# Optimization experiments

Hardware: AMD Instinct MI355X
Metric: run time of the kernel (lower is better)

The kernel has to match this reference:

```python
import jax, jax.numpy as jnp
import numpy as np

OS = 14            # output_size
GRID = 2           # ceil(roi_size/OS) = ceil(28/14) = 2 (boxes are built 28x28, sampling_ratio=-1)
NODES = OS * OS    # 196 graph nodes
EPS = 1e-5         # BatchNorm eps
K, B, C, H, W = 256, 4, 256, 112, 112


def _bn_relu(x, g, b, m, v):
    # eval-mode BatchNorm2d followed by ReLU (bn_act_conv prefix)
    s = jax.lax.rsqrt(v + EPS)
    xn = (x - m[None, :, None, None]) * s[None, :, None, None]
    return jax.nn.relu(xn * g[None, :, None, None] + b[None, :, None, None])


def _conv(x, w, b, pad):
    y = jax.lax.conv_general_dilated(x, w, (1, 1), [(pad, pad), (pad, pad)],
                                     dimension_numbers=('NCHW', 'OIHW', 'NCHW'))
    return y + b[None, :, None, None]


def _roi_align(sem, boxes):
    # torchvision roi_align, spatial_scale=1.0, aligned=False, sampling_ratio=-1 (static grid=2)
    Bs, Cc, Hh, Ww = sem.shape
    bidx = boxes[:, 0].astype(jnp.int32)
    x1, y1, x2, y2 = boxes[:, 1], boxes[:, 2], boxes[:, 3], boxes[:, 4]
    bw = jnp.maximum(x2 - x1, 1.0) / OS
    bh = jnp.maximum(y2 - y1, 1.0) / OS
    t = (jnp.arange(OS * GRID, dtype=sem.dtype) + 0.5) / GRID   # pw*GRID+ix collapsed
    xs = x1[:, None] + bw[:, None] * t                          # [K, 28]
    ys = y1[:, None] + bh[:, None] * t

    def prep(c, L):
        m = (c >= -1.0) & (c <= L)
        cc = jnp.clip(c, 0.0, L - 1)
        lo = jnp.floor(cc).astype(jnp.int32)
        hi = jnp.minimum(lo + 1, L - 1)
        return m, lo, hi, cc - lo

    my, yl, yh, ly = prep(ys, Hh)
    mx, xl, xh, lx = prep(xs, Ww)
    semt = jnp.transpose(sem, (0, 2, 3, 1))  # [B,H,W,C]

    def gat(ya, xa):
        return semt[bidx[:, None, None], ya[:, :, None], xa[:, None, :]]  # [K,28,28,C]

    ly_ = ly[:, :, None, None]
    lx_ = lx[:, None, :, None]
    val = (gat(yl, xl) * (1 - ly_) * (1 - lx_) + gat(yl, xh) * (1 - ly_) * lx_
           + gat(yh, xl) * ly_ * (1 - lx_) + gat(yh, xh) * ly_ * lx_)
    val = jnp.where((my[:, :, None] & mx[:, None, :])[..., None], val, 0.0)
    val = val.reshape(-1, OS, GRID, OS, GRID, Cc).mean(axis=(2, 4))  # avg over sampling grid
    return jnp.transpose(val, (0, 3, 1, 2))  # [K,C,14,14]


def _gcn_agg(A, x):
    # PyG gcn_norm on a fully-connected weighted graph (self loops already present):
    # deg[j] = sum_i A[i,j] (scatter on col); out[j] = sum_i d^-1/2[i] A[i,j] d^-1/2[j] x[i]
    deg = A.sum(axis=1)                 # [K,196]
    dis = jax.lax.rsqrt(deg)            # sigmoid weights > 0 => no zero degree
    Nrm = dis[:, :, None] * A * dis[:, None, :]
    return jnp.einsum('kij,kif->kjf', Nrm, x)


def _forward(roi_feature, semantic, boxes,
             bn_sem_g, bn_sem_b, bn_sem_m, bn_sem_v, conv_sem_w, conv_sem_b,
             bn_fpn_g, bn_fpn_b, bn_fpn_m, bn_fpn_v, conv_fpn_w, conv_fpn_b,
             bn_aff_g, bn_aff_b, bn_aff_m, bn_aff_v, conv_aff_w, conv_aff_b,
             gcn1_w, gcn1_b, gcn2_w, gcn2_b):
    roi_sem = _roi_align(semantic, boxes)                                   # [K,256,14,14]
    a = (_conv(_bn_relu(roi_sem, bn_sem_g, bn_sem_b, bn_sem_m, bn_sem_v), conv_sem_w, conv_sem_b, 1)
         + _conv(_bn_relu(roi_feature, bn_fpn_g, bn_fpn_b, bn_fpn_m, bn_fpn_v), conv_fpn_w, conv_fpn_b, 1))
    aff = _conv(_bn_relu(a, bn_aff_g, bn_aff_b, bn_aff_m, bn_aff_v), conv_aff_w, conv_aff_b, 0)
    A = jax.nn.sigmoid(aff.reshape(-1, NODES, NODES))                       # [K,196,196]
    X = roi_feature.reshape(-1, C, NODES).transpose(0, 2, 1)                # [K,196,256] node feats
    x1 = jax.nn.relu(_gcn_agg(A, X @ gcn1_w) + gcn1_b)                      # GCNConv(256,16)+ReLU
    x2 = _gcn_agg(A, x1 @ gcn2_w) + gcn2_b                                  # GCNConv(16,256)
    emb = x2.transpose(0, 2, 1).reshape(-1, C, OS, OS)
    return roi_sem + emb


def setup_inputs() -> dict:
    key = jax.random.key(0)
    ks = jax.random.split(key, 24)
    roi_feature = jax.random.normal(ks[0], (K, C, OS, OS), jnp.float32)
    semantic = jax.random.normal(ks[1], (B, C, H, W), jnp.float32)
    bidx = jax.random.randint(ks[2], (K,), 0, B).astype(jnp.float32)
    xy = jax.random.uniform(ks[3], (K, 2), jnp.float32, 0.0, float(H - 28))
    boxes = jnp.concatenate([bidx[:, None], xy, xy + 28.0], axis=1)  # (idx,x1,y1,x2,y2), 28x28 boxes

    def bn(kg, c):
        k1, k2, k3, k4 = jax.random.split(kg, 4)
        return (jax.random.normal(k1, (c,)) * 0.1 + 1.0,
                jax.random.normal(k2, (c,)) * 0.1,
                jax.random.normal(k3, (c,)) * 0.1,
                jax.random.uniform(k4, (c,), jnp.float32, 0.5, 1.5))
    bn_sem = bn(ks[4], C); bn_fpn = bn(ks[5], C); bn_aff = bn(ks[6], 64)
    inp = {
        'roi_feature': roi_feature, 'semantic': semantic, 'boxes': boxes,
        'bn_sem_g': bn_sem[0], 'bn_sem_b': bn_sem[1], 'bn_sem_m': bn_sem[2], 'bn_sem_v': bn_sem[3],
        'conv_sem_w': jax.random.normal(ks[7], (64, C, 3, 3)) * 0.02,
        'conv_sem_b': jax.random.normal(ks[8], (64,)) * 0.02,
        'bn_fpn_g': bn_fpn[0], 'bn_fpn_b': bn_fpn[1], 'bn_fpn_m': bn_fpn[2], 'bn_fpn_v': bn_fpn[3],
        'conv_fpn_w': jax.random.normal(ks[9], (64, C, 3, 3)) * 0.02,
        'conv_fpn_b': jax.random.normal(ks[10], (64,)) * 0.02,
        'bn_aff_g': bn_aff[0], 'bn_aff_b': bn_aff[1], 'bn_aff_m': bn_aff[2], 'bn_aff_v': bn_aff[3],
        'conv_aff_w': jax.random.normal(ks[11], (NODES, 64, 1, 1)) * 0.05,
        'conv_aff_b': jax.random.normal(ks[12], (NODES,)) * 0.05,
        'gcn1_w': jax.random.normal(ks[13], (C, 16)) * 0.05,
        'gcn1_b': jax.random.normal(ks[14], (16,)) * 0.05,
        'gcn2_w': jax.random.normal(ks[15], (16, C)) * 0.05,
        'gcn2_b': jax.random.normal(ks[16], (C,)) * 0.05,
    }
    return inp


def reference(roi_feature, semantic, boxes,
              bn_sem_g, bn_sem_b, bn_sem_m, bn_sem_v, conv_sem_w, conv_sem_b,
              bn_fpn_g, bn_fpn_b, bn_fpn_m, bn_fpn_v, conv_fpn_w, conv_fpn_b,
              bn_aff_g, bn_aff_b, bn_aff_m, bn_aff_v, conv_aff_w, conv_aff_b,
              gcn1_w, gcn1_b, gcn2_w, gcn2_b):
    return _forward(roi_feature, semantic, boxes,
                    bn_sem_g, bn_sem_b, bn_sem_m, bn_sem_v, conv_sem_w, conv_sem_b,
                    bn_fpn_g, bn_fpn_b, bn_fpn_m, bn_fpn_v, conv_fpn_w, conv_fpn_b,
                    bn_aff_g, bn_aff_b, bn_aff_m, bn_aff_v, conv_aff_w, conv_aff_b,
                    gcn1_w, gcn1_b, gcn2_w, gcn2_b)
```

## Files before the change

### kernel.cpp

```cpp
#include <hip/hip_runtime.h>
#include <hip/hip_bf16.h>

#define KBOX 256
#define CCH  256
#define NODES 196
#define OS 14
#define FTQ 3211264

typedef __attribute__((ext_vector_type(8))) short  bf16x8;
typedef __attribute__((ext_vector_type(8))) unsigned short u16x8;
typedef __attribute__((ext_vector_type(4))) float  f32x4;
typedef __attribute__((ext_vector_type(4))) short  s16x4;
typedef __attribute__((ext_vector_type(4))) int    i32x4;

__device__ __forceinline__ short f2bf(float x) {
  __hip_bfloat16 h = __float2bfloat16(x);
  return *reinterpret_cast<short*>(&h);
}
__device__ __forceinline__ float bf2f(unsigned short u) {
  unsigned int x = ((unsigned int)u) << 16;
  union { unsigned int i; float f; } c; c.i = x;
  return c.f;
}

#define MFMA16 __builtin_amdgcn_mfma_f32_16x16x32_bf16

__global__ __launch_bounds__(256) void prep_kernel(
    const float* __restrict__ bn_sem_g, const float* __restrict__ bn_sem_b,
    const float* __restrict__ bn_sem_m, const float* __restrict__ bn_sem_v,
    const float* __restrict__ conv_sem_w, const float* __restrict__ conv_sem_b,
    const float* __restrict__ bn_fpn_g, const float* __restrict__ bn_fpn_b,
    const float* __restrict__ bn_fpn_m, const float* __restrict__ bn_fpn_v,
    const float* __restrict__ conv_fpn_w, const float* __restrict__ conv_fpn_b,
    const float* __restrict__ bn_aff_g, const float* __restrict__ bn_aff_b,
    const float* __restrict__ bn_aff_m, const float* __restrict__ bn_aff_v,
    const float* __restrict__ conv_aff_w, const float* __restrict__ g1w,
    const float* __restrict__ g2w,
    float* __restrict__ ss_sem, float* __restrict__ ss_fpn, float* __restrict__ ss_aff2,
    short* __restrict__ wfrag, short* __restrict__ wafrag, short* __restrict__ g1wf,
    short* __restrict__ g2wf)
{
  int gid = blockIdx.x * blockDim.x + threadIdx.x;
  int gsz = gridDim.x * blockDim.x;
  for (int c = gid; c < 256; c += gsz) {
    float s = bn_sem_g[c] * rsqrtf(bn_sem_v[c] + 1e-5f);
    ss_sem[c] = s; ss_sem[256 + c] = bn_sem_b[c] - bn_sem_m[c] * s;
    float s2 = bn_fpn_g[c] * rsqrtf(bn_fpn_v[c] + 1e-5f);
    ss_fpn[c] = s2; ss_fpn[256 + c] = bn_fpn_b[c] - bn_fpn_m[c] * s2;
  }
  for (int c = gid; c < 64; c += gsz) {
    float s = bn_aff_g[c] * rsqrtf(bn_aff_v[c] + 1e-5f);
    float sh = bn_aff_b[c] - bn_aff_m[c] * s;
    float bias = conv_sem_b[c] + conv_fpn_b[c];
    ss_aff2[c] = s; ss_aff2[64 + c] = bias * s + sh;
  }
  for (int idx = gid; idx < 144 * 4 * 64 * 8; idx += gsz) {
    int e = idx & 7, lane = (idx >> 3) & 63, nt = (idx >> 9) & 3, kstep = idx >> 11;
    int src = kstep / 72, rem = kstep % 72, icc = rem / 9, pos = rem % 9;
    int ky = pos / 3, kx = pos % 3;
    int oc = nt * 16 + (lane & 15);
    int ic = icc * 32 + (lane >> 4) * 8 + e;
    const float* w = src ? conv_fpn_w : conv_sem_w;
    wfrag[idx] = f2bf(w[((oc * 256 + ic) * 3 + ky) * 3 + kx]);
  }
  for (int idx = gid; idx < 2 * 13 * 64 * 8; idx += gsz) {
    int t = idx;
    int e = t & 7; t >>= 3;
    int lane = t & 63; t >>= 6;
    int nt = t % 13; int s = t / 13;
    int i = nt * 16 + (lane & 15);
    int ic = s * 32 + (lane >> 4) * 8 + e;
    wafrag[idx] = f2bf(i < NODES ? conv_aff_w[i * 64 + ic] : 0.f);
  }
  for (int idx = gid; idx < 8 * 64 * 8; idx += gsz) {
    int e = idx & 7, lane = (idx >> 3) & 63, ks = idx >> 9;
    int ic = ks * 32 + (lane >> 4) * 8 + e;
    int f = lane & 15;
    g1wf[idx] = f2bf(g1w[ic * 16 + f]);
  }
  for (int idx = gid; idx < 16 * 64 * 8; idx += gsz) {
    int e = idx & 7, lane = (idx >> 3) & 63, ct = idx >> 9;
    int kk = (lane >> 4) * 8 + e;
    int c = ct * 16 + (lane & 15);
    g2wf[idx] = f2bf(kk < 16 ? g2w[kk * 256 + c] : 0.f);
  }
}

__global__ __launch_bounds__(256) void transpose_bf16_kernel(
    const float* __restrict__ in, unsigned short* __restrict__ out, int C, int HW)
{
  __shared__ float tile[64][65];
  int nh = (HW + 63) >> 6;
  int bi = blockIdx.x;
  int cb = bi % (C >> 6); bi /= (C >> 6);
  int hb = bi % nh; int b = bi / nh;
  int tx = threadIdx.x & 63, ty = threadIdx.x >> 6;
  const float* inb = in + (size_t)b * C * HW;
  unsigned short* outb = out + (size_t)b * HW * C;
  #pragma unroll
  for (int i = ty; i < 64; i += 4) {
    int c = cb * 64 + i, hw = hb * 64 + tx;
    tile[i][tx] = (hw < HW) ? inb[(size_t)c * HW + hw] : 0.f;
  }
  __syncthreads();
  int cp = threadIdx.x & 31;
  #pragma unroll
  for (int i = (int)(threadIdx.x >> 5); i < 64; i += 8) {
    int hw = hb * 64 + i;
    if (hw < HW) {
      ushort2 v;
      v.x = (unsigned short)f2bf(tile[cp * 2][i]);
      v.y = (unsigned short)f2bf(tile[cp * 2 + 1][i]);
      *(ushort2*)&outb[(size_t)hw * C + cb * 64 + cp * 2] = v;
    }
  }
}

__global__ __launch_bounds__(512) void roi_align_kernel(
    const unsigned short* __restrict__ semt, const float* __restrict__ boxes,
    unsigned short* __restrict__ roi_sem)
{
  __shared__ unsigned short slab[5][29][256];
  int kb = blockIdx.x / 7, g = blockIdx.x % 7;
  int tid = threadIdx.x, wave = tid >> 6, lane = tid & 63;
  const float* bx = boxes + kb * 5;
  int bb = (int)bx[0];
  float x1 = bx[1], y1 = bx[2];
  float xb = x1 + 0.5f, yv = y1 + 0.5f;
  int X0 = (int)floorf(xb); float fx = xb - (float)X0;
  int Y0 = (int)floorf(yv); float fy = yv - (float)Y0;
  const unsigned short* base = semt + (size_t)bb * 12544 * 256;
  #pragma unroll
  for (int i = 0; i < 19; ++i) {
    int s = wave + i * 8;
    if (s < 145) {
      int r = s / 29, xi = s - r * 29;
      int yr = min(Y0 + 4 * g + r, 111);
      int xc = min(X0 + xi, 111);
      *(s16x4*)&slab[r][xi][lane * 4] =
          *(const s16x4*)(base + ((size_t)yr * 112 + xc) * 256 + lane * 4);
    }
  }
  __syncthreads();
  int c2 = tid & 127, grp = tid >> 7;
  int oyl = grp >> 1, og = grp & 1;
  int rb = oyl * 2;
  float w0 = 1.f - fy;
  unsigned short* op = roi_sem + (((size_t)kb * NODES) + (2 * g + oyl) * OS) * 256 + c2 * 2;
  #pragma unroll
  for (int oxs = 0; oxs < 7; ++oxs) {
    int ox = og * 7 + oxs;
    float o0 = 0.f, o1 = 0.f;
    #pragma unroll
    for (int xi = 0; xi < 3; ++xi) {
      float xw = (xi == 0) ? (1.f - fx) : (xi == 1 ? 1.f : fx);
      const unsigned short* p0 = &slab[rb][2 * ox + xi][c2 * 2];
      const unsigned short* p1 = &slab[rb + 1][2 * ox + xi][c2 * 2];
      const unsigned short* p2 = &slab[rb + 2][2 * ox + xi][c2 * 2];
      o0 += xw * (w0 * bf2f(p0[0]) + bf2f(p1[0]) + fy * bf2f(p2[0]));
      o1 += xw * (w0 * bf2f(p0[1]) + bf2f(p1[1]) + fy * bf2f(p2[1]));
    }
    ushort2 v;
    v.x = (unsigned short)f2bf(o0 * 0.25f);
    v.y = (unsigned short)f2bf(o1 * 0.25f);
    *(ushort2*)(op + (size_t)ox * 256) = v;
  }
}

__global__ __launch_bounds__(256) void conv_ab_kernel(
    const unsigned short* __restrict__ roi_sem, const unsigned short* __restrict__ roif,
    const float* __restrict__ ss_sem, const float* __restrict__ ss_fpn,
    const short* __restrict__ wfrag, float* __restrict__ a_part)
{
  int bi = blockIdx.x;
  int k = bi >> 1, src = bi & 1;
  int tid = threadIdx.x;
  int wave = tid >> 6, lane = tid & 63;
  int l15 = lane & 15, lq = lane >> 4;
  __shared__ short lds_in[197][40];
  __shared__ short lds_wf[18432];
  __shared__ float lds_sc[256], lds_sh[256];

  {
    const float* ss = src ? ss_fpn : ss_sem;
    lds_sc[tid] = ss[tid]; lds_sh[tid] = ss[256 + tid];
  }
  if (tid < 40) lds_in[196][tid] = 0;

  int oyA[4], oxA[4], jA[4]; bool mvA[4];
  #pragma unroll
  for (int mi = 0; mi < 4; ++mi) {
    int mt = (mi < 3) ? (wave + mi * 4) : 12;
    mvA[mi] = (mi < 3) | (wave == 3);
    int j = mt * 16 + l15;
    jA[mi] = j;
    int oy = j / 14;
    oyA[mi] = oy; oxA[mi] = j - oy * 14;
  }

  u16x8 inv[4];
  i32x4 wv[9];
  const unsigned short* inp = (src ? roif : roi_sem) + (size_t)k * NODES * CCH;
  const short* wbase = wfrag + (size_t)src * 72 * 2048;

  f32x4 acc[4][4];
  #pragma unroll
  for (int i = 0; i < 4; ++i)
    #pragma unroll
    for (int j = 0; j < 4; ++j) acc[i][j] = f32x4{0.f, 0.f, 0.f, 0.f};

#define ISSUE_LOADS(P) do {                                                  \
    int icc_ = (P);                                                          \
    const unsigned short* in_ = inp + icc_ * 32;                             \
    _Pragma("unroll")                                                        \
    for (int i_ = 0; i_ < 3; ++i_) {                                         \
      int f_ = tid + i_ * 256;                                               \
      inv[i_] = *(const u16x8*)(in_ + (size_t)(f_ >> 2) * 256 + (f_ & 3) * 8); \
    }                                                                        \
    if (tid < 16) {                                                          \
      int f_ = 768 + tid;                                                    \
      inv[3] = *(const u16x8*)(in_ + (size_t)(f_ >> 2) * 256 + (f_ & 3) * 8); \
    }                                                                        \
    const i32x4* wsl_ = (const i32x4*)(wbase + (size_t)icc_ * 9 * 2048);     \
    _Pragma("unroll")                                                        \
    for (int i_ = 0; i_ < 9; ++i_) wv[i_] = wsl_[tid + i_ * 256];            \
  } while (0)

#define WRITE_STAGE(P) do {                                                  \
    int icc_ = (P);                                                          \
    _Pragma("unroll")                                                        \
    for (int i_ = 0; i_ < 3; ++i_) {                                         \
      int f_ = tid + i_ * 256;                                               \
      int j_ = f_ >> 2, cq_ = f_ & 3;                                        \
      bf16x8 pk_;                                                            \
      _Pragma("unroll")                                                      \
      for (int u_ = 0; u_ < 8; ++u_) {                                       \
        int c_ = icc_ * 32 + cq_ * 8 + u_;                                   \
        float x_ = bf2f(inv[i_][u_]) * lds_sc[c_] + lds_sh[c_];              \
        pk_[u_] = f2bf(fmaxf(x_, 0.f));                                      \
      }                                                                      \
      *(bf16x8*)&lds_in[j_][cq_ * 8] = pk_;                                  \
    }                                                                        \
    if (tid < 16) {                                                          \
      int f_ = 768 + tid; int j_ = f_ >> 2, cq_ = f_ & 3;                    \
      bf16x8 pk_;                                                            \
      _Pragma("unroll")                                                      \
      for (int u_ = 0; u_ < 8; ++u_) {                                       \
        int c_ = icc_ * 32 + cq_ * 8 + u_;                                   \
        float x_ = bf2f(inv[3][u_]) * lds_sc[c_] + lds_sh[c_];               \
        pk_[u_] = f2bf(fmaxf(x_, 0.f));                                      \
      }                                                                      \
      *(bf16x8*)&lds_in[j_][cq_ * 8] = pk_;                                  \
    }                                                                        \
    _Pragma("unroll")                                                        \
    for (int i_ = 0; i_ < 9; ++i_) ((i32x4*)lds_wf)[tid + i_ * 256] = wv[i_];\
  } while (0)

  ISSUE_LOADS(0);
  __syncthreads();
  WRITE_STAGE(0);

  for (int p = 0; p < 8; ++p) {
    __syncthreads();
    if (p < 7) ISSUE_LOADS(p + 1);
    #pragma unroll
    for (int pos = 0; pos < 9; ++pos) {
      int ky = pos / 3 - 1, kx = pos % 3 - 1;
      bf16x8 bfr[4];
      #pragma unroll
      for (int n = 0; n < 4; ++n)
        bfr[n] = *(const bf16x8*)&lds_wf[((pos * 4 + n) * 64 + lane) * 8];
      #pragma unroll
      for (int mi = 0; mi < 4; ++mi) {
        if (!mvA[mi]) continue;
        int ny = oyA[mi] + ky, nx = oxA[mi] + kx;
        bool v = (jA[mi] < 196) & ((unsigned)ny < 14u) & ((unsigned)nx < 14u);
        int np = v ? (ny * 14 + nx) : 196;
        bf16x8 afr = *(const bf16x8*)&lds_in[np][lq * 8];
        acc[mi][0] = MFMA16(afr, bfr[0], acc[mi][0], 0, 0, 0);
        acc[mi][1] = MFMA16(afr, bfr[1], acc[mi][1], 0, 0, 0);
        acc[mi][2] = MFMA16(afr, bfr[2], acc[mi][2], 0, 0, 0);
        acc[mi][3] = MFMA16(afr, bfr[3], acc[mi][3], 0, 0, 0);
      }
    }
    __syncthreads();
    if (p < 7) WRITE_STAGE(p + 1);
  }

  float* op = a_part + (size_t)src * FTQ;
  #pragma unroll
  for (int mi = 0; mi < 4; ++mi) {
    if (!mvA[mi]) continue;
    int mt = (mi < 3) ? (wave + mi * 4) : 12;
    #pragma unroll
    for (int n = 0; n < 4; ++n) {
      int oc = n * 16 + l15;
      #pragma unroll
      for (int r = 0; r < 4; ++r) {
        int j = mt * 16 + lq * 4 + r;
        if (j < NODES)
          op[((size_t)k * NODES + j) * 64 + oc] = acc[mi][n][r];
      }
    }
  }
#undef ISSUE_LOADS
#undef WRITE_STAGE
}

__global__ __launch_bounds__(1024, 1) void graph_kernel(
    const float* __restrict__ a_part, const float* __restrict__ ss_aff2,
    const short* __restrict__ wafrag,
    const float* __restrict__ aff_b, const short* __restrict__ g1wf,
    const float* __restrict__ g1b, const unsigned short* __restrict__ roif_bf,
    const short* __restrict__ g2wf, const float* __restrict__ g2b,
    const unsigned short* __restrict__ roi_sem, float* __restrict__ outp)
{
  __shared__ __align__(16) char smem[125840];
  const int tid = threadIdx.x, wave = tid >> 6, lane = tid & 63;
  const int l15 = lane & 15, lq = lane >> 4;
  const int k = blockIdx.x;

  char*  Ab   = smem;
  short* wa   = (short*)(smem + 96512);
  short* yfr  = (short*)(smem + 96512);
  short* zsf  = (short*)(smem + 103680);
  float* dsl  = (float*)(smem + 123136);
  float* g1bl = (float*)(smem + 123968);
  float* g2bl = (float*)(smem + 124032);
  float* affb = (float*)(smem + 125056);

  const bool wv13 = (wave < 13);
  const int jr  = wave * 16 + l15;
  const int jrc = min(jr, 195);
  const i32x4 z4 = {};

  bf16x8 af0 = {}, af1 = {};
  if (wv13) {
    const float* p0 = a_part + ((size_t)k * NODES + jrc) * 64 + lq * 8;
    const float* p1 = p0 + FTQ;
    f32x4 a00 = *(const f32x4*)p0;
    f32x4 a01 = *(const f32x4*)(p0 + 4);
    f32x4 a02 = *(const f32x4*)(p0 + 32);
    f32x4 a03 = *(const f32x4*)(p0 + 36);
    f32x4 b00 = *(const f32x4*)p1;
    f32x4 b01 = *(const f32x4*)(p1 + 4);
    f32x4 b02 = *(const f32x4*)(p1 + 32);
    f32x4 b03 = *(const f32x4*)(p1 + 36);
    f32x4 sc0a = *(const f32x4*)(ss_aff2 + lq * 8);
    f32x4 sc0b = *(const f32x4*)(ss_aff2 + lq * 8 + 4);
    f32x4 sc1a = *(const f32x4*)(ss_aff2 + 32 + lq * 8);
    f32x4 sc1b = *(const f32x4*)(ss_aff2 + 32 + lq * 8 + 4);
    f32x4 sh0a = *(const f32x4*)(ss_aff2 + 64 + lq * 8);
    f32x4 sh0b = *(const f32x4*)(ss_aff2 + 64 + lq * 8 + 4);
    f32x4 sh1a = *(const f32x4*)(ss_aff2 + 96 + lq * 8);
    f32x4 sh1b = *(const f32x4*)(ss_aff2 + 96 + lq * 8 + 4);
    #pragma unroll
    for (int e = 0; e < 4; ++e) {
      af0[e]     = f2bf(fmaxf((a00[e] + b00[e]) * sc0a[e] + sh0a[e], 0.f));
      af0[e + 4] = f2bf(fmaxf((a01[e] + b01[e]) * sc0b[e] + sh0b[e], 0.f));
      af1[e]     = f2bf(fmaxf((a02[e] + b02[e]) * sc1a[e] + sh1a[e], 0.f));
      af1[e + 4] = f2bf(fmaxf((a03[e] + b03[e]) * sc1b[e] + sh1b[e], 0.f));
    }
  }
  {
    i32x4 w0 = ((const i32x4*)wafrag)[tid];
    i32x4 w1 = z4;
    if (tid < 640) w1 = ((const i32x4*)wafrag)[1024 + tid];
    if (tid < 832) {
      int r = tid >> 2, q = tid & 3;
      *(i32x4*)(Ab + r * 464 + 384 + q * 16) = z4;
    }
    if (tid < 196) affb[tid] = aff_b[tid];
    if (tid < 256) g2bl[tid] = g2b[tid];
    if (tid < 16)  g1bl[tid] = g1b[tid];
    ((i32x4*)wa)[tid] = w0;
    if (tid < 640) ((i32x4*)wa)[1024 + tid] = w1;
  }
  __syncthreads();

  if (wv13) {
    float rsum[4] = {0.f, 0.f, 0.f, 0.f};
    #pragma unroll
    for (int n = 0; n < 13; ++n) {
      bf16x8 b0 = *(const bf16x8*)(wa + (n * 64 + lane) * 8);
      bf16x8 b1 = *(const bf16x8*)(wa + ((13 + n) * 64 + lane) * 8);
      f32x4 acc = {0.f, 0.f, 0.f, 0.f};
      acc = MFMA16(af0, b0, acc, 0, 0, 0);
      acc = MFMA16(af1, b1, acc, 0, 0, 0);
      int i = n * 16 + l15;
      bool iv = (i < 196);
      float bv = affb[iv ? i : 0];
      #pragma unroll
      for (int r = 0; r < 4; ++r) {
        float v = acc[r] + bv;
        float s = 1.f / (1.f + __expf(-v));
        if (iv) {
          rsum[r] += s;
          *(short*)(Ab + (wave * 16 + lq * 4 + r) * 464 + i * 2) = f2bf(s);
        }
      }
    }
    #pragma unroll
    for (int r = 0; r < 4; ++r) {
      float v = rsum[r];
      v += __shfl_xor(v, 1); v += __shfl_xor(v, 2);
      v += __shfl_xor(v, 4); v += __shfl_xor(v, 8);
      int j = wave * 16 + lq * 4 + r;
      if (l15 == 0 && j < 196) dsl[j] = rsqrtf(v);
    }
  }
  __syncthreads();

  *(i32x4*)(smem + 96512 + tid * 16) = z4;
  if (tid < 256) *(i32x4*)(smem + 96512 + (1024 + tid) * 16) = z4;
  f32x4 xacc = {0.f, 0.f, 0.f, 0.f};
  if (wv13) {
    const unsigned short* Xp = roif_bf + (size_t)k * 50176 + (size_t)jrc * 256 + lq * 8;
    #pragma unroll
    for (int ks = 0; ks < 8; ++ks) {
      bf16x8 xa = *(const bf16x8*)(Xp + ks * 32);
      bf16x8 xb = *(const bf16x8*)(g1wf + (ks * 64 + lane) * 8);
      xacc = MFMA16(xa, xb, xacc, 0, 0, 0);
    }
  }
  __syncthreads();

  if (wv13) {
    #pragma unroll
    for (int r = 0; r < 4; ++r) {
      int i = wave * 16 + lq * 4 + r;
      if (i < 196) {
        float yv = dsl[i] * xacc[r];
        yfr[((i >> 5) * 64 + ((i >> 3) & 3) * 16 + l15) * 8 + (i & 7)] = f2bf(yv);
      }
    }
  }
  __syncthreads();

  f32x4 g0 = {0.f, 0.f, 0.f, 0.f};
  if (wv13) {
    #pragma unroll
    for (int ks = 0; ks < 7; ++ks) {
      bf16x8 bb = *(const bf16x8*)(yfr + (ks * 64 + lane) * 8);
      bf16x8 a0 = *(const bf16x8*)(Ab + jr * 464 + ks * 64 + lq * 16);
      g0 = MFMA16(a0, bb, g0, 0, 0, 0);
    }
  }
  __syncthreads();
  if (wv13) {
    #pragma unroll
    for (int r = 0; r < 4; ++r) {
      int i = wave * 16 + lq * 4 + r;
      if (i < 196) {
        float d = dsl[i];
        float x1v = fmaxf(g0[r] * d + g1bl[l15], 0.f);
        yfr[((i >> 5) * 64 + ((i >> 3) & 3) * 16 + l15) * 8 + (i & 7)] = f2bf(d * x1v);
      }
    }
  }
  __syncthreads();

  if (wv13) {
    f32x4 z0 = {0.f, 0.f, 0.f, 0.f};
    #pragma unroll
    for (int ks = 0; ks < 7; ++ks) {
      bf16x8 bb = *(const bf16x8*)(yfr + (ks * 64 + lane) * 8);
      bf16x8 a0 = *(const bf16x8*)(Ab + jr * 464 + ks * 64 + lq * 16);
      z0 = MFMA16(a0, bb, z0, 0, 0, 0);
    }
    #pragma unroll
    for (int r = 0; r < 4; ++r) {
      int j = wave * 16 + lq * 4 + r;
      if (j < 196) {
        float zv = z0[r] * dsl[j];
        zsf[((j >> 4) * 64 + (l15 >> 3) * 16 + (j & 15)) * 8 + (l15 & 7)] = f2bf(zv);
      }
    }
  }
  __syncthreads();

  {
    bf16x8 wf = *(const bf16x8*)(g2wf + (wave * 64 + lane) * 8);
    const unsigned short* rsmk = roi_sem + (size_t)k * 50176;
    float* op = outp + (size_t)k * 50176;
    float gbv[4];
    #pragma unroll
    for (int r = 0; r < 4; ++r) gbv[r] = g2bl[wave * 16 + lq * 4 + r];
    #pragma unroll
    for (int jt = 0; jt < 13; ++jt) {
      bf16x8 zb = *(const bf16x8*)(zsf + (jt * 64 + lane) * 8);
      f32x4 d = {0.f, 0.f, 0.f, 0.f};
      d = MFMA16(wf, zb, d, 0, 0, 0);
      int j = jt * 16 + l15;
      if (j < 196) {
        #pragma unroll
        for (int r = 0; r < 4; ++r) {
          int c = wave * 16 + lq * 4 + r;
          op[(size_t)c * 196 + j] = d[r] + gbv[r] + bf2f(rsmk[(size_t)j * 256 + c]);
        }
      }
    }
  }
}

extern "C" void kernel_launch(void* const* d_in, const int* in_sizes, int n_in,
                              void* d_out, int out_size, void* d_ws, size_t ws_size,
                              hipStream_t stream) {
  const float* roi_feature = (const float*)d_in[0];
  const float* semantic    = (const float*)d_in[1];
  const float* boxes       = (const float*)d_in[2];
  const float* bn_sem_g = (const float*)d_in[3];
  const float* bn_sem_b = (const float*)d_in[4];
  const float* bn_sem_m = (const float*)d_in[5];
  const float* bn_sem_v = (const float*)d_in[6];
  const float* conv_sem_w = (const float*)d_in[7];
  const float* conv_sem_b = (const float*)d_in[8];
  const float* bn_fpn_g = (const float*)d_in[9];
  const float* bn_fpn_b = (const float*)d_in[10];
  const float* bn_fpn_m = (const float*)d_in[11];
  const float* bn_fpn_v = (const float*)d_in[12];
  const float* conv_fpn_w = (const float*)d_in[13];
  const float* conv_fpn_b = (const float*)d_in[14];
  const float* bn_aff_g = (const float*)d_in[15];
  const float* bn_aff_b = (const float*)d_in[16];
  const float* bn_aff_m = (const float*)d_in[17];
  const float* bn_aff_v = (const float*)d_in[18];
  const float* conv_aff_w = (const float*)d_in[19];
  const float* conv_aff_b = (const float*)d_in[20];
  const float* gcn1_w = (const float*)d_in[21];
  const float* gcn1_b = (const float*)d_in[22];
  const float* gcn2_w = (const float*)d_in[23];
  const float* gcn2_b = (const float*)d_in[24];

  const size_t FT = (size_t)KBOX * NODES * CCH;
  unsigned short* ws16      = (unsigned short*)d_ws;
  unsigned short* semt_bf   = ws16;
  unsigned short* roif_bf   = semt_bf + FT;
  unsigned short* roi_sem_b = roif_bf + FT;
  float*          a_part    = (float*)(roi_sem_b + FT);
  float*          ss_sem    = a_part + 2 * (size_t)FTQ;
  float*          ss_fpn    = ss_sem + 512;
  float*          ss_aff2   = ss_fpn + 512;
  short*          wfrag     = (short*)(ss_aff2 + 128);
  short*          wafrag    = wfrag + 294912;
  short*          g1wf      = wafrag + 13312;
  short*          g2wf      = g1wf + 4096;

  prep_kernel<<<256, 256, 0, stream>>>(
      bn_sem_g, bn_sem_b, bn_sem_m, bn_sem_v, conv_sem_w, conv_sem_b,
      bn_fpn_g, bn_fpn_b, bn_fpn_m, bn_fpn_v, conv_fpn_w, conv_fpn_b,
      bn_aff_g, bn_aff_b, bn_aff_m, bn_aff_v, conv_aff_w, gcn1_w, gcn2_w,
      ss_sem, ss_fpn, ss_aff2, wfrag, wafrag, g1wf, g2wf);

  transpose_bf16_kernel<<<4 * 196 * 4, 256, 0, stream>>>(semantic, semt_bf, 256, 12544);
  transpose_bf16_kernel<<<4 * 4 * 256, 256, 0, stream>>>(roi_feature, roif_bf, 256, 196);
  roi_align_kernel<<<KBOX * 7, 512, 0, stream>>>(semt_bf, boxes, roi_sem_b);
  conv_ab_kernel<<<KBOX * 2, 256, 0, stream>>>(roi_sem_b, roif_bf, ss_sem, ss_fpn, wfrag, a_part);
  graph_kernel<<<KBOX, 1024, 0, stream>>>(a_part, ss_aff2, wafrag, conv_aff_b, g1wf, gcn1_b,
                                          roif_bf, g2wf, gcn2_b, roi_sem_b, (float*)d_out);
}
```

Baseline: 140.2 us.

## Split conv input channels across blocks, store bf16 partials, stage residual in LDS

The conv kernel now splits the 256 input channels into two halves handled by separate blocks, doubling the grid to 1024 blocks. It writes four bf16 partial sums instead of two fp32 ones, and the graph kernel adds them before BN/ReLU. The LDS input row stride changes from 40 to 36 shorts, presumably to cut bank conflicts. The graph kernel's final residual add now stages roi_sem rows into shared memory with coalesced loads instead of strided global reads. Rounding partials to bf16 adds error, and the partial buffer gains an extra reduction pass.

```diff
diff --git a/kernel.cpp b/kernel.cpp
--- a/kernel.cpp
+++ b/kernel.cpp
@@ -170,14 +170,14 @@
 __global__ __launch_bounds__(256) void conv_ab_kernel(
     const unsigned short* __restrict__ roi_sem, const unsigned short* __restrict__ roif,
     const float* __restrict__ ss_sem, const float* __restrict__ ss_fpn,
-    const short* __restrict__ wfrag, float* __restrict__ a_part)
+    const short* __restrict__ wfrag, short* __restrict__ a_part)
 {
   int bi = blockIdx.x;
-  int k = bi >> 1, src = bi & 1;
+  int k = bi >> 2, src = (bi >> 1) & 1, ih = bi & 1;
   int tid = threadIdx.x;
   int wave = tid >> 6, lane = tid & 63;
   int l15 = lane & 15, lq = lane >> 4;
-  __shared__ short lds_in[197][40];
+  __shared__ short lds_in[197 * 36 + 4];
   __shared__ short lds_wf[18432];
   __shared__ float lds_sc[256], lds_sh[256];
 
@@ -185,7 +185,7 @@
     const float* ss = src ? ss_fpn : ss_sem;
     lds_sc[tid] = ss[tid]; lds_sh[tid] = ss[256 + tid];
   }
-  if (tid < 40) lds_in[196][tid] = 0;
+  if (tid < 36) lds_in[196 * 36 + tid] = 0;
 
   int oyA[4], oxA[4], jA[4]; bool mvA[4];
   #pragma unroll
@@ -201,7 +201,6 @@
   u16x8 inv[4];
   i32x4 wv[9];
   const unsigned short* inp = (src ? roif : roi_sem) + (size_t)k * NODES * CCH;
-  const short* wbase = wfrag + (size_t)src * 72 * 2048;
 
   f32x4 acc[4][4];
   #pragma unroll
@@ -210,7 +209,7 @@
     for (int j = 0; j < 4; ++j) acc[i][j] = f32x4{0.f, 0.f, 0.f, 0.f};
 
 #define ISSUE_LOADS(P) do {                                                  \
-    int icc_ = (P);                                                          \
+    int icc_ = ih * 4 + (P);                                                 \
     const unsigned short* in_ = inp + icc_ * 32;                             \
     _Pragma("unroll")                                                        \
     for (int i_ = 0; i_ < 3; ++i_) {                                         \
@@ -221,13 +220,13 @@
       int f_ = 768 + tid;                                                    \
       inv[3] = *(const u16x8*)(in_ + (size_t)(f_ >> 2) * 256 + (f_ & 3) * 8); \
     }                                                                        \
-    const i32x4* wsl_ = (const i32x4*)(wbase + (size_t)icc_ * 9 * 2048);     \
+    const i32x4* wsl_ = (const i32x4*)(wfrag + (size_t)(src * 72 + icc_ * 9) * 2048); \
     _Pragma("unroll")                                                        \
     for (int i_ = 0; i_ < 9; ++i_) wv[i_] = wsl_[tid + i_ * 256];            \
   } while (0)
 
 #define WRITE_STAGE(P) do {                                                  \
-    int icc_ = (P);                                                          \
+    int icc_ = ih * 4 + (P);                                                 \
     _Pragma("unroll")                                                        \
     for (int i_ = 0; i_ < 3; ++i_) {                                         \
       int f_ = tid + i_ * 256;                                               \
@@ -239,7 +238,7 @@
         float x_ = bf2f(inv[i_][u_]) * lds_sc[c_] + lds_sh[c_];              \
         pk_[u_] = f2bf(fmaxf(x_, 0.f));                                      \
       }                                                                      \
-      *(bf16x8*)&lds_in[j_][cq_ * 8] = pk_;                                  \
+      *(bf16x8*)&lds_in[j_ * 36 + cq_ * 8] = pk_;                            \
     }                                                                        \
     if (tid < 16) {                                                          \
       int f_ = 768 + tid; int j_ = f_ >> 2, cq_ = f_ & 3;                    \
@@ -250,7 +249,7 @@
         float x_ = bf2f(inv[3][u_]) * lds_sc[c_] + lds_sh[c_];               \
         pk_[u_] = f2bf(fmaxf(x_, 0.f));                                      \
       }                                                                      \
-      *(bf16x8*)&lds_in[j_][cq_ * 8] = pk_;                                  \
+      *(bf16x8*)&lds_in[j_ * 36 + cq_ * 8] = pk_;                            \
     }                                                                        \
     _Pragma("unroll")                                                        \
     for (int i_ = 0; i_ < 9; ++i_) ((i32x4*)lds_wf)[tid + i_ * 256] = wv[i_];\
@@ -260,9 +259,9 @@
   __syncthreads();
   WRITE_STAGE(0);
 
-  for (int p = 0; p < 8; ++p) {
+  for (int p = 0; p < 4; ++p) {
     __syncthreads();
-    if (p < 7) ISSUE_LOADS(p + 1);
+    if (p < 3) ISSUE_LOADS(p + 1);
     #pragma unroll
     for (int pos = 0; pos < 9; ++pos) {
       int ky = pos / 3 - 1, kx = pos % 3 - 1;
@@ -276,7 +275,7 @@
         int ny = oyA[mi] + ky, nx = oxA[mi] + kx;
         bool v = (jA[mi] < 196) & ((unsigned)ny < 14u) & ((unsigned)nx < 14u);
         int np = v ? (ny * 14 + nx) : 196;
-        bf16x8 afr = *(const bf16x8*)&lds_in[np][lq * 8];
+        bf16x8 afr = *(const bf16x8*)&lds_in[np * 36 + lq * 8];
         acc[mi][0] = MFMA16(afr, bfr[0], acc[mi][0], 0, 0, 0);
         acc[mi][1] = MFMA16(afr, bfr[1], acc[mi][1], 0, 0, 0);
         acc[mi][2] = MFMA16(afr, bfr[2], acc[mi][2], 0, 0, 0);
@@ -284,10 +283,10 @@
       }
     }
     __syncthreads();
-    if (p < 7) WRITE_STAGE(p + 1);
-  }
-
-  float* op = a_part + (size_t)src * FTQ;
+    if (p < 3) WRITE_STAGE(p + 1);
+  }
+
+  short* op = a_part + (size_t)(src * 2 + ih) * FTQ;
   #pragma unroll
   for (int mi = 0; mi < 4; ++mi) {
     if (!mvA[mi]) continue;
@@ -299,7 +298,7 @@
       for (int r = 0; r < 4; ++r) {
         int j = mt * 16 + lq * 4 + r;
         if (j < NODES)
-          op[((size_t)k * NODES + j) * 64 + oc] = acc[mi][n][r];
+          op[((size_t)k * NODES + j) * 64 + oc] = f2bf(acc[mi][n][r]);
       }
     }
   }
@@ -308,7 +307,7 @@
 }
 
 __global__ __launch_bounds__(1024, 1) void graph_kernel(
-    const float* __restrict__ a_part, const float* __restrict__ ss_aff2,
+    const short* __restrict__ a_part, const float* __restrict__ ss_aff2,
     const short* __restrict__ wafrag,
     const float* __restrict__ aff_b, const short* __restrict__ g1wf,
     const float* __restrict__ g1b, const unsigned short* __restrict__ roif_bf,
@@ -336,30 +335,21 @@
 
   bf16x8 af0 = {}, af1 = {};
   if (wv13) {
-    const float* p0 = a_part + ((size_t)k * NODES + jrc) * 64 + lq * 8;
-    const float* p1 = p0 + FTQ;
-    f32x4 a00 = *(const f32x4*)p0;
-    f32x4 a01 = *(const f32x4*)(p0 + 4);
-    f32x4 a02 = *(const f32x4*)(p0 + 32);
-    f32x4 a03 = *(const f32x4*)(p0 + 36);
-    f32x4 b00 = *(const f32x4*)p1;
-    f32x4 b01 = *(const f32x4*)(p1 + 4);
-    f32x4 b02 = *(const f32x4*)(p1 + 32);
-    f32x4 b03 = *(const f32x4*)(p1 + 36);
-    f32x4 sc0a = *(const f32x4*)(ss_aff2 + lq * 8);
-    f32x4 sc0b = *(const f32x4*)(ss_aff2 + lq * 8 + 4);
-    f32x4 sc1a = *(const f32x4*)(ss_aff2 + 32 + lq * 8);
-    f32x4 sc1b = *(const f32x4*)(ss_aff2 + 32 + lq * 8 + 4);
-    f32x4 sh0a = *(const f32x4*)(ss_aff2 + 64 + lq * 8);
-    f32x4 sh0b = *(const f32x4*)(ss_aff2 + 64 + lq * 8 + 4);
-    f32x4 sh1a = *(const f32x4*)(ss_aff2 + 96 + lq * 8);
-    f32x4 sh1b = *(const f32x4*)(ss_aff2 + 96 + lq * 8 + 4);
-    #pragma unroll
-    for (int e = 0; e < 4; ++e) {
-      af0[e]     = f2bf(fmaxf((a00[e] + b00[e]) * sc0a[e] + sh0a[e], 0.f));
-      af0[e + 4] = f2bf(fmaxf((a01[e] + b01[e]) * sc0b[e] + sh0b[e], 0.f));
-      af1[e]     = f2bf(fmaxf((a02[e] + b02[e]) * sc1a[e] + sh1a[e], 0.f));
-      af1[e + 4] = f2bf(fmaxf((a03[e] + b03[e]) * sc1b[e] + sh1b[e], 0.f));
+    float s0[8] = {0,0,0,0,0,0,0,0}, s1[8] = {0,0,0,0,0,0,0,0};
+    #pragma unroll
+    for (int sl = 0; sl < 4; ++sl) {
+      const unsigned short* p = (const unsigned short*)a_part + (size_t)sl * FTQ
+                                + ((size_t)k * NODES + jrc) * 64 + lq * 8;
+      u16x8 v0 = *(const u16x8*)p;
+      u16x8 v1 = *(const u16x8*)(p + 32);
+      #pragma unroll
+      for (int e = 0; e < 8; ++e) { s0[e] += bf2f(v0[e]); s1[e] += bf2f(v1[e]); }
+    }
+    #pragma unroll
+    for (int e = 0; e < 8; ++e) {
+      int oc0 = lq * 8 + e, oc1 = 32 + lq * 8 + e;
+      af0[e] = f2bf(fmaxf(s0[e] * ss_aff2[oc0] + ss_aff2[64 + oc0], 0.f));
+      af1[e] = f2bf(fmaxf(s1[e] * ss_aff2[oc1] + ss_aff2[64 + oc1], 0.f));
     }
   }
   {
@@ -483,21 +473,56 @@
     bf16x8 wf = *(const bf16x8*)(g2wf + (wave * 64 + lane) * 8);
     const unsigned short* rsmk = roi_sem + (size_t)k * 50176;
     float* op = outp + (size_t)k * 50176;
+    unsigned short* rst = (unsigned short*)smem;
+    const int c_ = wave * 16 + lq * 4;
     float gbv[4];
     #pragma unroll
-    for (int r = 0; r < 4; ++r) gbv[r] = g2bl[wave * 16 + lq * 4 + r];
-    #pragma unroll
-    for (int jt = 0; jt < 13; ++jt) {
+    for (int r = 0; r < 4; ++r) gbv[r] = g2bl[c_ + r];
+    #pragma unroll
+    for (int it = 0; it < 3; ++it) {
+      int v = tid + it * 1024;
+      int row = v >> 5, cq = v & 31;
+      *(u16x8*)&rst[row * 264 + cq * 8] = *(const u16x8*)(rsmk + (size_t)row * 256 + cq * 8);
+    }
+    __syncthreads();
+    #pragma unroll
+    for (int jt = 0; jt < 6; ++jt) {
+      bf16x8 zb = *(const bf16x8*)(zsf + (jt * 64 + lane) * 8);
+      f32x4 d = {0.f, 0.f, 0.f, 0.f};
+      d = MFMA16(wf, zb, d, 0, 0, 0);
+      int j = jt * 16 + l15;
+      const unsigned short* rr = rst + j * 264 + c_;
+      unsigned int p01 = *(const unsigned int*)rr;
+      unsigned int p23 = *(const unsigned int*)(rr + 2);
+      op[(size_t)(c_ + 0) * 196 + j] = d[0] + gbv[0] + bf2f((unsigned short)(p01 & 0xffff));
+      op[(size_t)(c_ + 1) * 196 + j] = d[1] + gbv[1] + bf2f((unsigned short)(p01 >> 16));
+      op[(size_t)(c_ + 2) * 196 + j] = d[2] + gbv[2] + bf2f((unsigned short)(p23 & 0xffff));
+      op[(size_t)(c_ + 3) * 196 + j] = d[3] + gbv[3] + bf2f((unsigned short)(p23 >> 16));
+    }
+    __syncthreads();
+    #pragma unroll
+    for (int it = 0; it < 4; ++it) {
+      int v = tid + it * 1024;
+      if (v < 3200) {
+        int row = v >> 5, cq = v & 31;
+        *(u16x8*)&rst[row * 264 + cq * 8] = *(const u16x8*)(rsmk + (size_t)(96 + row) * 256 + cq * 8);
+      }
+    }
+    __syncthreads();
+    #pragma unroll
+    for (int jt = 6; jt < 13; ++jt) {
       bf16x8 zb = *(const bf16x8*)(zsf + (jt * 64 + lane) * 8);
       f32x4 d = {0.f, 0.f, 0.f, 0.f};
       d = MFMA16(wf, zb, d, 0, 0, 0);
       int j = jt * 16 + l15;
       if (j < 196) {
-        #pragma unroll
-        for (int r = 0; r < 4; ++r) {
-          int c = wave * 16 + lq * 4 + r;
-          op[(size_t)c * 196 + j] = d[r] + gbv[r] + bf2f(rsmk[(size_t)j * 256 + c]);
-        }
+        const unsigned short* rr = rst + (j - 96) * 264 + c_;
+        unsigned int p01 = *(const unsigned int*)rr;
+        unsigned int p23 = *(const unsigned int*)(rr + 2);
+        op[(size_t)(c_ + 0) * 196 + j] = d[0] + gbv[0] + bf2f((unsigned short)(p01 & 0xffff));
+        op[(size_t)(c_ + 1) * 196 + j] = d[1] + gbv[1] + bf2f((unsigned short)(p01 >> 16));
+        op[(size_t)(c_ + 2) * 196 + j] = d[2] + gbv[2] + bf2f((unsigned short)(p23 & 0xffff));
+        op[(size_t)(c_ + 3) * 196 + j] = d[3] + gbv[3] + bf2f((unsigned short)(p23 >> 16));
       }
     }
   }
@@ -537,8 +562,8 @@
   unsigned short* semt_bf   = ws16;
   unsigned short* roif_bf   = semt_bf + FT;
   unsigned short* roi_sem_b = roif_bf + FT;
-  float*          a_part    = (float*)(roi_sem_b + FT);
-  float*          ss_sem    = a_part + 2 * (size_t)FTQ;
+  short*          a_part    = (short*)(roi_sem_b + FT);
+  float*          ss_sem    = (float*)(a_part + 4 * (size_t)FTQ);
   float*          ss_fpn    = ss_sem + 512;
   float*          ss_aff2   = ss_fpn + 512;
   short*          wfrag     = (short*)(ss_aff2 + 128);
@@ -555,7 +580,7 @@
   transpose_bf16_kernel<<<4 * 196 * 4, 256, 0, stream>>>(semantic, semt_bf, 256, 12544);
   transpose_bf16_kernel<<<4 * 4 * 256, 256, 0, stream>>>(roi_feature, roif_bf, 256, 196);
   roi_align_kernel<<<KBOX * 7, 512, 0, stream>>>(semt_bf, boxes, roi_sem_b);
-  conv_ab_kernel<<<KBOX * 2, 256, 0, stream>>>(roi_sem_b, roif_bf, ss_sem, ss_fpn, wfrag, a_part);
+  conv_ab_kernel<<<KBOX * 4, 256, 0, stream>>>(roi_sem_b, roif_bf, ss_sem, ss_fpn, wfrag, a_part);
   graph_kernel<<<KBOX, 1024, 0, stream>>>(a_part, ss_aff2, wafrag, conv_aff_b, g1wf, gcn1_b,
                                           roif_bf, g2wf, gcn2_b, roi_sem_b, (float*)d_out);
 }
```

Measured after the change: 145.3 us. 1.04x slower.
